# Kernel tuning notes

Measured on AMD Instinct MI355X. Metric: run time of the kernel, lower is better.

## Reference

```python
import jax, jax.numpy as jnp
import numpy as np

N_NODES = 50000
N_EDGES = 800000
D_IN = 128
D_OUT = 128


def setup_inputs() -> dict:
    key = jax.random.key(0)
    k1, k2, k3, k4, k5 = jax.random.split(key, 5)
    feature = jax.random.normal(k1, (N_NODES, D_IN), dtype=jnp.float32)
    src = jax.random.randint(k2, (N_EDGES,), 0, N_NODES, dtype=jnp.int32)
    dst = jax.random.randint(k3, (N_EDGES,), 0, N_NODES, dtype=jnp.int32)
    # nn.Linear-style init: U(-1/sqrt(in), 1/sqrt(in))
    bound = 1.0 / np.sqrt(D_IN)
    W = jax.random.uniform(k4, (D_OUT, D_IN), minval=-bound, maxval=bound, dtype=jnp.float32)
    b = jax.random.uniform(k5, (D_OUT,), minval=-bound, maxval=bound, dtype=jnp.float32)
    return {"feature": feature, "src": src, "dst": dst, "W": W, "b": b}


def reference(feature, src, dst, W, b):
    # copy_src: gather source node features along edges, then sum-reduce per dst
    msgs = feature[src]                                    # [E, D_IN]
    h = jax.ops.segment_sum(msgs, dst, num_segments=N_NODES)  # [N, D_IN]
    # linear projection: h @ W^T + b
    return jnp.einsum("nd,od->no", h, W) + b               # [N, D_OUT]
```

## Files before the change

kernel.cpp:

```cpp
#include <hip/hip_runtime.h>
#include <hip/hip_bf16.h>


#define BKT_SHIFT 6
#define MAX_BKT   800
#define NPART     128
#define CAP       1280
#define NCAP      64

typedef __attribute__((ext_vector_type(8))) short short8;
typedef __attribute__((ext_vector_type(4))) float float4v;

__device__ __forceinline__ unsigned short f2bf_rne(float f) {
    unsigned int u = __float_as_uint(f);
    u += 0x7FFFu + ((u >> 16) & 1u);
    return (unsigned short)(u >> 16);
}

__global__ __launch_bounds__(512) void conv_scatter_kernel(
    const float* __restrict__ feat, const float* __restrict__ W,
    unsigned short* __restrict__ out_bf, long nf, long nw,
    const int* __restrict__ src, const int* __restrict__ dst,
    int* __restrict__ cursor, unsigned int* __restrict__ pairs,
    int n_edges, int nb, int chunk)
{
    if ((int)blockIdx.x < NPART) {
        __shared__ int lcnt[MAX_BKT];
        __shared__ int lcur[MAX_BKT];
        int tid = threadIdx.x;
        int p   = blockIdx.x;
        int e0  = p * chunk;
        int e1  = min(e0 + chunk, n_edges);
        int cnt = e1 - e0;
        int nfull = cnt >> 2;

        for (int i = tid; i < nb; i += 512) lcnt[i] = 0;
        __syncthreads();
        for (int k = tid; k < nfull; k += 512) {
            int4 d4 = *(const int4*)(dst + e0 + k * 4);
            atomicAdd(&lcnt[d4.x >> BKT_SHIFT], 1);
            atomicAdd(&lcnt[d4.y >> BKT_SHIFT], 1);
            atomicAdd(&lcnt[d4.z >> BKT_SHIFT], 1);
            atomicAdd(&lcnt[d4.w >> BKT_SHIFT], 1);
        }
        for (int e = e0 + nfull * 4 + tid; e < e1; e += 512)
            atomicAdd(&lcnt[dst[e] >> BKT_SHIFT], 1);
        __syncthreads();
        for (int i = tid; i < nb; i += 512) {
            int c = lcnt[i];
            int base = c ? atomicAdd(&cursor[i], c) : 0;
            lcur[i] = i * CAP + base;
        }
        __syncthreads();
        for (int k = tid; k < nfull; k += 512) {
            int4 d4 = *(const int4*)(dst + e0 + k * 4);
            int4 s4 = *(const int4*)(src + e0 + k * 4);
            int p0 = atomicAdd(&lcur[d4.x >> BKT_SHIFT], 1);
            pairs[p0] = ((unsigned)(d4.x & 63) << 20) | (unsigned)s4.x;
            int p1 = atomicAdd(&lcur[d4.y >> BKT_SHIFT], 1);
            pairs[p1] = ((unsigned)(d4.y & 63) << 20) | (unsigned)s4.y;
            int p2 = atomicAdd(&lcur[d4.z >> BKT_SHIFT], 1);
            pairs[p2] = ((unsigned)(d4.z & 63) << 20) | (unsigned)s4.z;
            int p3 = atomicAdd(&lcur[d4.w >> BKT_SHIFT], 1);
            pairs[p3] = ((unsigned)(d4.w & 63) << 20) | (unsigned)s4.w;
        }
        for (int e = e0 + nfull * 4 + tid; e < e1; e += 512) {
            int d = dst[e];
            int pos = atomicAdd(&lcur[d >> BKT_SHIFT], 1);
            pairs[pos] = ((unsigned)(d & 63) << 20) | (unsigned)src[e];
        }
    } else {
        long i4 = ((long)(blockIdx.x - NPART) * 512 + threadIdx.x) * 4;
        if (i4 >= nf + nw) return;
        const float* srcp = (i4 < nf) ? (feat + i4) : (W + (i4 - nf));
        float4 v = *(const float4*)srcp;
        ushort4 o;
        o.x = f2bf_rne(v.x); o.y = f2bf_rne(v.y);
        o.z = f2bf_rne(v.z); o.w = f2bf_rne(v.w);
        *(ushort4*)(out_bf + i4) = o;
    }
}

#define HT_STRIDE 136

#define ACC8(U)                                                     \
    do {                                                            \
        acc[0] += __uint_as_float((U).x << 16);                     \
        acc[1] += __uint_as_float((U).x & 0xFFFF0000u);             \
        acc[2] += __uint_as_float((U).y << 16);                     \
        acc[3] += __uint_as_float((U).y & 0xFFFF0000u);             \
        acc[4] += __uint_as_float((U).z << 16);                     \
        acc[5] += __uint_as_float((U).z & 0xFFFF0000u);             \
        acc[6] += __uint_as_float((U).w << 16);                     \
        acc[7] += __uint_as_float((U).w & 0xFFFF0000u);             \
    } while (0)

__global__ __launch_bounds__(1024, 8) void gcn_gather_mm_kernel(
    const unsigned short* __restrict__ feat_bf,
    const unsigned int* __restrict__ pairs, const int* __restrict__ cursor,
    const unsigned short* __restrict__ w_bf, const float* __restrict__ bias,
    float* __restrict__ out, int n_nodes)
{
    __shared__ unsigned short htile[64 * HT_STRIDE];
    __shared__ int lst[64][NCAP];
    __shared__ int lcnt[64];

    int tid   = threadIdx.x;
    int lane  = tid & 63;
    int w     = tid >> 6;
    int node0 = blockIdx.x << 6;
    int sub   = lane >> 4;
    int c16   = lane & 15;

    int bucket = blockIdx.x;
    int bstart = bucket * CAP;
    int bcnt   = min(cursor[bucket], CAP);

    if (tid < 64) lcnt[tid] = 0;
    __syncthreads();
    for (int i = tid; i < bcnt; i += 1024) {
        unsigned int pr = pairs[bstart + i];
        int local = (int)(pr >> 20);
        int pos = atomicAdd(&lcnt[local], 1);
        if (pos < NCAP) lst[local][pos] = (int)(pr & 0xFFFFFu);
    }
    __syncthreads();

    const unsigned short* colp = feat_bf + c16 * 8;

    #pragma unroll
    for (int i = 0; i < 4; i++) {
        int loc = (w << 2) + i;
        float acc[8];
        #pragma unroll
        for (int j = 0; j < 8; j++) acc[j] = 0.f;

        int deg = (node0 + loc < n_nodes) ? min(lcnt[loc], NCAP) : 0;
        if (deg > 0) {
            int sv = (lane < deg) ? lst[loc][lane] : 0;
            int g = 0;
            for (; g + 16 <= deg; g += 16) {
                int sa = __shfl(sv, g + sub);
                int sb = __shfl(sv, g + 4 + sub);
                int sc = __shfl(sv, g + 8 + sub);
                int sd = __shfl(sv, g + 12 + sub);
                uint4 ua = *(const uint4*)(colp + (size_t)sa * 128);
                uint4 ub = *(const uint4*)(colp + (size_t)sb * 128);
                uint4 uc = *(const uint4*)(colp + (size_t)sc * 128);
                uint4 ud = *(const uint4*)(colp + (size_t)sd * 128);
                ACC8(ua); ACC8(ub); ACC8(uc); ACC8(ud);
            }
            for (; g + 4 <= deg; g += 4) {
                int s0 = __shfl(sv, g + sub);
                uint4 u = *(const uint4*)(colp + (size_t)s0 * 128);
                ACC8(u);
            }
            if (g < deg) {
                int rem = deg - g;
                int idx = g + (sub < rem ? sub : rem - 1);
                int s = __shfl(sv, idx);
                uint4 u = *(const uint4*)(colp + (size_t)s * 128);
                if (sub < rem) ACC8(u);
            }
            #pragma unroll
            for (int j = 0; j < 8; j++) {
                acc[j] += __shfl_xor(acc[j], 16);
                acc[j] += __shfl_xor(acc[j], 32);
            }
        }

        if (sub == 0) {
            short8 o;
            #pragma unroll
            for (int j = 0; j < 8; j++) o[j] = (short)f2bf_rne(acc[j]);
            *(short8*)(htile + loc * HT_STRIDE + c16 * 8) = o;
        }
    }

    __syncthreads();

    int m = lane & 15;
    int q = lane >> 4;

    #pragma unroll
    for (int pp = w; pp < 32; pp += 16) {
        int mt = pp >> 3;
        int nt = pp & 7;

        float4v accd = {0.f, 0.f, 0.f, 0.f};
        #pragma unroll
        for (int kk = 0; kk < 4; kk++) {
            short8 afrag = *(const short8*)(htile + (mt * 16 + m) * HT_STRIDE + kk * 32 + q * 8);
            short8 bfrag = *(const short8*)(w_bf + (size_t)(nt * 16 + m) * 128 + kk * 32 + q * 8);
            accd = __builtin_amdgcn_mfma_f32_16x16x32_bf16(afrag, bfrag, accd, 0, 0, 0);
        }
        float bv = bias[nt * 16 + m];
        #pragma unroll
        for (int r = 0; r < 4; r++) {
            int row = node0 + mt * 16 + q * 4 + r;
            if (row < n_nodes)
                out[(size_t)row * 128 + nt * 16 + m] = accd[r] + bv;
        }
    }
}

extern "C" void kernel_launch(void* const* d_in, const int* in_sizes, int n_in,
                              void* d_out, int out_size, void* d_ws, size_t ws_size,
                              hipStream_t stream) {
    const float* feature = (const float*)d_in[0];
    const int*   src     = (const int*)d_in[1];
    const int*   dst     = (const int*)d_in[2];
    const float* W       = (const float*)d_in[3];
    const float* b       = (const float*)d_in[4];

    const int D  = 128;
    int n_nodes  = in_sizes[0] / D;
    int n_edges  = in_sizes[1];
    int nb       = (n_nodes + 63) >> BKT_SHIFT;

    float* out = (float*)d_out;

    long nf = (long)n_nodes * D;
    long nw = (long)D * D;

    unsigned short* bf_base    = (unsigned short*)d_ws;
    unsigned short* feature_bf = bf_base;
    unsigned short* w_bf       = bf_base + nf;
    unsigned int* pairs  = (unsigned int*)(bf_base + nf + nw);
    int*          cursor = (int*)(pairs + (size_t)nb * CAP);

    int chunk = (n_edges + NPART - 1) / NPART;

    hipMemsetAsync(cursor, 0, (size_t)nb * sizeof(int), stream);

    {
        long conv_blocks = ((nf + nw) / 4 + 511) / 512;
        int grid = NPART + (int)conv_blocks;
        conv_scatter_kernel<<<grid, 512, 0, stream>>>(
            feature, W, bf_base, nf, nw, src, dst, cursor, pairs,
            n_edges, nb, chunk);
    }

    {
        gcn_gather_mm_kernel<<<nb, 1024, 0, stream>>>(
            feature_bf, pairs, cursor, w_bf, b, out, n_nodes);
    }
}
```

Baseline: 136.2 us.

## Halve bucket size and interleave four node gathers per wave for memory parallelism

Buckets now cover 32 nodes instead of 64, so the gather+MMA kernel runs with 512 threads per block across twice as many blocks and uses less shared memory per block. Each wave now gathers its four nodes together, issuing up to four independent row loads per iteration so more memory requests are in flight, where before it handled one node at a time. The cost is more accumulator registers, more per-iteration predication, and smaller MMA tiles per block. The scatter partition histogram also grows to 1600 buckets with a smaller per-bucket capacity, which raises the risk of overflowing a bucket.

```diff
diff --git a/kernel.cpp b/kernel.cpp
--- a/kernel.cpp
+++ b/kernel.cpp
@@ -2,10 +2,10 @@
 #include <hip/hip_bf16.h>
 
 
-#define BKT_SHIFT 6
-#define MAX_BKT   800
+#define BKT_SHIFT 5
+#define MAX_BKT   1600
 #define NPART     128
-#define CAP       1280
+#define CAP       768
 #define NCAP      64
 
 typedef __attribute__((ext_vector_type(8))) short short8;
@@ -56,18 +56,18 @@
             int4 d4 = *(const int4*)(dst + e0 + k * 4);
             int4 s4 = *(const int4*)(src + e0 + k * 4);
             int p0 = atomicAdd(&lcur[d4.x >> BKT_SHIFT], 1);
-            pairs[p0] = ((unsigned)(d4.x & 63) << 20) | (unsigned)s4.x;
+            pairs[p0] = ((unsigned)(d4.x & 31) << 20) | (unsigned)s4.x;
             int p1 = atomicAdd(&lcur[d4.y >> BKT_SHIFT], 1);
-            pairs[p1] = ((unsigned)(d4.y & 63) << 20) | (unsigned)s4.y;
+            pairs[p1] = ((unsigned)(d4.y & 31) << 20) | (unsigned)s4.y;
             int p2 = atomicAdd(&lcur[d4.z >> BKT_SHIFT], 1);
-            pairs[p2] = ((unsigned)(d4.z & 63) << 20) | (unsigned)s4.z;
+            pairs[p2] = ((unsigned)(d4.z & 31) << 20) | (unsigned)s4.z;
             int p3 = atomicAdd(&lcur[d4.w >> BKT_SHIFT], 1);
-            pairs[p3] = ((unsigned)(d4.w & 63) << 20) | (unsigned)s4.w;
+            pairs[p3] = ((unsigned)(d4.w & 31) << 20) | (unsigned)s4.w;
         }
         for (int e = e0 + nfull * 4 + tid; e < e1; e += 512) {
             int d = dst[e];
             int pos = atomicAdd(&lcur[d >> BKT_SHIFT], 1);
-            pairs[pos] = ((unsigned)(d & 63) << 20) | (unsigned)src[e];
+            pairs[pos] = ((unsigned)(d & 31) << 20) | (unsigned)src[e];
         }
     } else {
         long i4 = ((long)(blockIdx.x - NPART) * 512 + threadIdx.x) * 4;
@@ -83,32 +83,32 @@
 
 #define HT_STRIDE 136
 
-#define ACC8(U)                                                     \
+#define ACC8(A, U)                                                  \
     do {                                                            \
-        acc[0] += __uint_as_float((U).x << 16);                     \
-        acc[1] += __uint_as_float((U).x & 0xFFFF0000u);             \
-        acc[2] += __uint_as_float((U).y << 16);                     \
-        acc[3] += __uint_as_float((U).y & 0xFFFF0000u);             \
-        acc[4] += __uint_as_float((U).z << 16);                     \
-        acc[5] += __uint_as_float((U).z & 0xFFFF0000u);             \
-        acc[6] += __uint_as_float((U).w << 16);                     \
-        acc[7] += __uint_as_float((U).w & 0xFFFF0000u);             \
+        A[0] += __uint_as_float((U).x << 16);                       \
+        A[1] += __uint_as_float((U).x & 0xFFFF0000u);               \
+        A[2] += __uint_as_float((U).y << 16);                       \
+        A[3] += __uint_as_float((U).y & 0xFFFF0000u);               \
+        A[4] += __uint_as_float((U).z << 16);                       \
+        A[5] += __uint_as_float((U).z & 0xFFFF0000u);               \
+        A[6] += __uint_as_float((U).w << 16);                       \
+        A[7] += __uint_as_float((U).w & 0xFFFF0000u);               \
     } while (0)
 
-__global__ __launch_bounds__(1024, 8) void gcn_gather_mm_kernel(
+__global__ __launch_bounds__(512, 8) void gcn_gather_mm_kernel(
     const unsigned short* __restrict__ feat_bf,
     const unsigned int* __restrict__ pairs, const int* __restrict__ cursor,
     const unsigned short* __restrict__ w_bf, const float* __restrict__ bias,
     float* __restrict__ out, int n_nodes)
 {
-    __shared__ unsigned short htile[64 * HT_STRIDE];
-    __shared__ int lst[64][NCAP];
-    __shared__ int lcnt[64];
+    __shared__ unsigned short htile[32 * HT_STRIDE];
+    __shared__ int lst[32][NCAP];
+    __shared__ int lcnt[32];
 
     int tid   = threadIdx.x;
     int lane  = tid & 63;
     int w     = tid >> 6;
-    int node0 = blockIdx.x << 6;
+    int node0 = blockIdx.x << 5;
     int sub   = lane >> 4;
     int c16   = lane & 15;
 
@@ -116,9 +116,9 @@
     int bstart = bucket * CAP;
     int bcnt   = min(cursor[bucket], CAP);
 
-    if (tid < 64) lcnt[tid] = 0;
+    if (tid < 32) lcnt[tid] = 0;
     __syncthreads();
-    for (int i = tid; i < bcnt; i += 1024) {
+    for (int i = tid; i < bcnt; i += 512) {
         unsigned int pr = pairs[bstart + i];
         int local = (int)(pr >> 20);
         int pos = atomicAdd(&lcnt[local], 1);
@@ -127,54 +127,78 @@
     __syncthreads();
 
     const unsigned short* colp = feat_bf + c16 * 8;
-
+    int bl = w << 2;
+
+    float acc0[8], acc1[8], acc2[8], acc3[8];
     #pragma unroll
-    for (int i = 0; i < 4; i++) {
-        int loc = (w << 2) + i;
-        float acc[8];
+    for (int j = 0; j < 8; j++) {
+        acc0[j] = 0.f; acc1[j] = 0.f; acc2[j] = 0.f; acc3[j] = 0.f;
+    }
+
+    int d0 = __builtin_amdgcn_readfirstlane(
+        (node0 + bl + 0 < n_nodes) ? min(lcnt[bl + 0], NCAP) : 0);
+    int d1 = __builtin_amdgcn_readfirstlane(
+        (node0 + bl + 1 < n_nodes) ? min(lcnt[bl + 1], NCAP) : 0);
+    int d2 = __builtin_amdgcn_readfirstlane(
+        (node0 + bl + 2 < n_nodes) ? min(lcnt[bl + 2], NCAP) : 0);
+    int d3 = __builtin_amdgcn_readfirstlane(
+        (node0 + bl + 3 < n_nodes) ? min(lcnt[bl + 3], NCAP) : 0);
+
+    int sv0 = lst[bl + 0][lane];
+    int sv1 = lst[bl + 1][lane];
+    int sv2 = lst[bl + 2][lane];
+    int sv3 = lst[bl + 3][lane];
+
+    int g0 = (d0 + 3) >> 2, g1 = (d1 + 3) >> 2;
+    int g2 = (d2 + 3) >> 2, g3 = (d3 + 3) >> 2;
+    int gmax = max(max(g0, g1), max(g2, g3));
+
+    for (int r = 0; r < gmax; ++r) {
+        int row = (r << 2) + sub;
+        uint4 u0 = {0,0,0,0}, u1 = {0,0,0,0}, u2 = {0,0,0,0}, u3 = {0,0,0,0};
+        if (r < g0) {
+            int sr = __shfl(sv0, min(row, d0 - 1));
+            u0 = *(const uint4*)(colp + (size_t)sr * 128);
+        }
+        if (r < g1) {
+            int sr = __shfl(sv1, min(row, d1 - 1));
+            u1 = *(const uint4*)(colp + (size_t)sr * 128);
+        }
+        if (r < g2) {
+            int sr = __shfl(sv2, min(row, d2 - 1));
+            u2 = *(const uint4*)(colp + (size_t)sr * 128);
+        }
+        if (r < g3) {
+            int sr = __shfl(sv3, min(row, d3 - 1));
+            u3 = *(const uint4*)(colp + (size_t)sr * 128);
+        }
+        if (r < g0 && row < d0) ACC8(acc0, u0);
+        if (r < g1 && row < d1) ACC8(acc1, u1);
+        if (r < g2 && row < d2) ACC8(acc2, u2);
+        if (r < g3 && row < d3) ACC8(acc3, u3);
+    }
+
+    #pragma unroll
+    for (int j = 0; j < 8; j++) {
+        acc0[j] += __shfl_xor(acc0[j], 16); acc0[j] += __shfl_xor(acc0[j], 32);
+        acc1[j] += __shfl_xor(acc1[j], 16); acc1[j] += __shfl_xor(acc1[j], 32);
+        acc2[j] += __shfl_xor(acc2[j], 16); acc2[j] += __shfl_xor(acc2[j], 32);
+        acc3[j] += __shfl_xor(acc3[j], 16); acc3[j] += __shfl_xor(acc3[j], 32);
+    }
+
+    if (sub == 0) {
+        short8 o0, o1, o2, o3;
         #pragma unroll
-        for (int j = 0; j < 8; j++) acc[j] = 0.f;
-
-        int deg = (node0 + loc < n_nodes) ? min(lcnt[loc], NCAP) : 0;
-        if (deg > 0) {
-            int sv = (lane < deg) ? lst[loc][lane] : 0;
-            int g = 0;
-            for (; g + 16 <= deg; g += 16) {
-                int sa = __shfl(sv, g + sub);
-                int sb = __shfl(sv, g + 4 + sub);
-                int sc = __shfl(sv, g + 8 + sub);
-                int sd = __shfl(sv, g + 12 + sub);
-                uint4 ua = *(const uint4*)(colp + (size_t)sa * 128);
-                uint4 ub = *(const uint4*)(colp + (size_t)sb * 128);
-                uint4 uc = *(const uint4*)(colp + (size_t)sc * 128);
-                uint4 ud = *(const uint4*)(colp + (size_t)sd * 128);
-                ACC8(ua); ACC8(ub); ACC8(uc); ACC8(ud);
-            }
-            for (; g + 4 <= deg; g += 4) {
-                int s0 = __shfl(sv, g + sub);
-                uint4 u = *(const uint4*)(colp + (size_t)s0 * 128);
-                ACC8(u);
-            }
-            if (g < deg) {
-                int rem = deg - g;
-                int idx = g + (sub < rem ? sub : rem - 1);
-                int s = __shfl(sv, idx);
-                uint4 u = *(const uint4*)(colp + (size_t)s * 128);
-                if (sub < rem) ACC8(u);
-            }
-            #pragma unroll
-            for (int j = 0; j < 8; j++) {
-                acc[j] += __shfl_xor(acc[j], 16);
-                acc[j] += __shfl_xor(acc[j], 32);
-            }
-        }
-
-        if (sub == 0) {
-            short8 o;
-            #pragma unroll
-            for (int j = 0; j < 8; j++) o[j] = (short)f2bf_rne(acc[j]);
-            *(short8*)(htile + loc * HT_STRIDE + c16 * 8) = o;
-        }
+        for (int j = 0; j < 8; j++) {
+            o0[j] = (short)f2bf_rne(acc0[j]);
+            o1[j] = (short)f2bf_rne(acc1[j]);
+            o2[j] = (short)f2bf_rne(acc2[j]);
+            o3[j] = (short)f2bf_rne(acc3[j]);
+        }
+        *(short8*)(htile + (bl + 0) * HT_STRIDE + c16 * 8) = o0;
+        *(short8*)(htile + (bl + 1) * HT_STRIDE + c16 * 8) = o1;
+        *(short8*)(htile + (bl + 2) * HT_STRIDE + c16 * 8) = o2;
+        *(short8*)(htile + (bl + 3) * HT_STRIDE + c16 * 8) = o3;
     }
 
     __syncthreads();
@@ -183,7 +207,7 @@
     int q = lane >> 4;
 
     #pragma unroll
-    for (int pp = w; pp < 32; pp += 16) {
+    for (int pp = w; pp < 16; pp += 8) {
         int mt = pp >> 3;
         int nt = pp & 7;
 
@@ -216,7 +240,7 @@
     const int D  = 128;
     int n_nodes  = in_sizes[0] / D;
     int n_edges  = in_sizes[1];
-    int nb       = (n_nodes + 63) >> BKT_SHIFT;
+    int nb       = (n_nodes + 31) >> BKT_SHIFT;
 
     float* out = (float*)d_out;
 
@@ -242,7 +266,7 @@
     }
 
     {
-        gcn_gather_mm_kernel<<<nb, 1024, 0, stream>>>(
+        gcn_gather_mm_kernel<<<nb, 512, 0, stream>>>(
             feature_bf, pairs, cursor, w_bf, b, out, n_nodes);
     }
 }
```

New measurement: 145.5 us. 1.07x slower.
